# Kernel tuning notes

Measured on AMD Instinct MI355X. Metric: run time of the kernel, lower is better.

The kernel has to match this reference:

```python
import math
import jax, jax.numpy as jnp
import numpy as np

N_HEADS = 32
N_KV_HEADS = 8
HEAD_DIM = 128
DIM = 4096
B = 32
MAX_SEQ = 4096
Q_LEN = 1
START_POS = 4095


def setup_inputs() -> dict:
    key = jax.random.key(0)
    ks = jax.random.split(key, 9)
    x = jax.random.normal(ks[0], (B, Q_LEN, DIM), dtype=jnp.float32)
    # RoPE angles for the current positions (seqlen=Q_LEN, half head_dim pairs)
    inv_freq = 1.0 / (500000.0 ** (np.arange(0, HEAD_DIM, 2, dtype=np.float32) / HEAD_DIM))
    pos = np.arange(START_POS, START_POS + Q_LEN, dtype=np.float32)
    ang = pos[:, None] * inv_freq[None, :]  # [Q_LEN, HEAD_DIM//2]
    freqs_cos = jnp.asarray(np.cos(ang), dtype=jnp.float32)
    freqs_sin = jnp.asarray(np.sin(ang), dtype=jnp.float32)
    cache_k = jax.random.normal(ks[1], (B, MAX_SEQ, N_KV_HEADS, HEAD_DIM), dtype=jnp.float32)
    cache_v = jax.random.normal(ks[2], (B, MAX_SEQ, N_KV_HEADS, HEAD_DIM), dtype=jnp.float32)
    s = 0.02
    wq = jax.random.normal(ks[3], (N_HEADS * HEAD_DIM, DIM), dtype=jnp.float32) * s
    wk = jax.random.normal(ks[4], (N_KV_HEADS * HEAD_DIM, DIM), dtype=jnp.float32) * s
    wv = jax.random.normal(ks[5], (N_KV_HEADS * HEAD_DIM, DIM), dtype=jnp.float32) * s
    wo = jax.random.normal(ks[6], (DIM, N_HEADS * HEAD_DIM), dtype=jnp.float32) * s
    return {"x": x, "start_pos": START_POS, "freqs_cos": freqs_cos, "freqs_sin": freqs_sin,
            "cache_k": cache_k, "cache_v": cache_v, "wq": wq, "wk": wk, "wv": wv, "wo": wo}


def _rope(t, cos, sin):
    # t: [B, S, h, hd]; cos/sin: [S, hd//2]; complex multiply on (even, odd) pairs
    tr = t.reshape(*t.shape[:-1], HEAD_DIM // 2, 2)
    a, b = tr[..., 0], tr[..., 1]
    c = cos[None, :, None, :]
    s = sin[None, :, None, :]
    out = jnp.stack([a * c - b * s, a * s + b * c], axis=-1)
    return out.reshape(t.shape)


def reference(x, start_pos, freqs_cos, freqs_sin, cache_k, cache_v, wq, wk, wv, wo):
    bsz, seqlen, _ = x.shape
    n_rep = N_HEADS // N_KV_HEADS
    xq = jnp.einsum('bsd,od->bso', x, wq).reshape(bsz, seqlen, N_HEADS, HEAD_DIM)
    xk = jnp.einsum('bsd,od->bso', x, wk).reshape(bsz, seqlen, N_KV_HEADS, HEAD_DIM)
    xv = jnp.einsum('bsd,od->bso', x, wv).reshape(bsz, seqlen, N_KV_HEADS, HEAD_DIM)
    xq = _rope(xq, freqs_cos, freqs_sin)
    xk = _rope(xk, freqs_cos, freqs_sin)
    # KV-cache update (start_pos is a static Python int)
    cache_k = cache_k.at[:, start_pos:start_pos + seqlen].set(xk)
    cache_v = cache_v.at[:, start_pos:start_pos + seqlen].set(xv)
    keys = cache_k[:, :start_pos + seqlen]    # [B, T, Hkv, hd]
    values = cache_v[:, :start_pos + seqlen]  # [B, T, Hkv, hd]
    # GQA: group query heads [H] -> [Hkv, n_rep]; avoids materializing repeated KV
    q = xq.reshape(bsz, seqlen, N_KV_HEADS, n_rep, HEAD_DIM)
    scale = 1.0 / math.sqrt(HEAD_DIM)
    scores = jnp.einsum('bsgrd,btgd->bgrst', q, keys) * scale  # [B, Hkv, n_rep, S, T]
    probs = jax.nn.softmax(scores, axis=-1)
    out = jnp.einsum('bgrst,btgd->bsgrd', probs, values)
    out = out.reshape(bsz, seqlen, N_HEADS * HEAD_DIM)
    return jnp.einsum('bse,de->bsd', out, wo)
```

## Files before the change

### kernel.cpp

```cpp
#include <hip/hip_runtime.h>

#define B_    32
#define DIM_  4096
#define NH_   32
#define NKV_  8
#define HD_   128
#define TSEQ  4096
#define NQKV  6144
#define GSPLIT 32
#define BK    32
#define NT    128
#define KRANGE (DIM_ / GSPLIT)
#define KTILES (KRANGE / BK)
#define TSPL  32
#define TS    128

typedef float f4_t __attribute__((ext_vector_type(4)));

__device__ __forceinline__ f4_t ntl(const float* p) {
    return __builtin_nontemporal_load((const f4_t*)p);
}

template<int CTRL>
__device__ __forceinline__ float dpp_add(float x) {
    const int y = __builtin_amdgcn_update_dpp(0, __float_as_int(x),
                                              CTRL, 0xF, 0xF, true);
    return x + __int_as_float(y);
}
__device__ __forceinline__ float red32(float x) {
    x = dpp_add<0xB1>(x);
    x = dpp_add<0x4E>(x);
    x = dpp_add<0x141>(x);
    x = dpp_add<0x140>(x);
    x += __shfl_xor(x, 16);
    return x;
}

__global__ __launch_bounds__(256) void gemm32(
    const float* __restrict__ A, const float* __restrict__ w0,
    const float* __restrict__ w1, const float* __restrict__ w2,
    int b1, int b2, int N, float* __restrict__ po)
{
    __shared__ __align__(16) float wt[BK][NT + 4];
    __shared__ __align__(16) float xp[KRANGE][33];
    const int tid = threadIdx.x;
    const int cg  = tid & 31;
    const int bg  = tid >> 5;
    const int ct  = blockIdx.x * NT;
    const int k0  = blockIdx.y * KRANGE;

    const float* wb_; int c0_;
    if (ct < b1)      { wb_ = w0; c0_ = ct; }
    else if (ct < b2) { wb_ = w1; c0_ = ct - b1; }
    else              { wb_ = w2; c0_ = ct - b2; }

    const int kqx = (tid & 31) * 4;
    const int rrx = tid >> 5;
    const int kq2 = (tid & 7) * 4;
    const int rr2 = tid >> 3;

    f4_t wreg[4];

    #pragma unroll
    for (int st = 0; st < 4; ++st) {
        const int bb = st * 8 + rrx;
        const f4_t xv = *(const f4_t*)(A + (size_t)bb * DIM_ + k0 + kqx);
        xp[kqx + 0][bb] = xv[0]; xp[kqx + 1][bb] = xv[1];
        xp[kqx + 2][bb] = xv[2]; xp[kqx + 3][bb] = xv[3];
    }
    #pragma unroll
    for (int st = 0; st < 4; ++st)
        wreg[st] = ntl(wb_ + (size_t)(c0_ + st * 32 + rr2) * DIM_ + k0 + kq2);
    #pragma unroll
    for (int st = 0; st < 4; ++st) {
        const int c = st * 32 + rr2;
        wt[kq2 + 0][c] = wreg[st][0]; wt[kq2 + 1][c] = wreg[st][1];
        wt[kq2 + 2][c] = wreg[st][2]; wt[kq2 + 3][c] = wreg[st][3];
    }
    __syncthreads();

    float acc[4][4];
    #pragma unroll
    for (int i = 0; i < 4; ++i)
        #pragma unroll
        for (int j = 0; j < 4; ++j) acc[i][j] = 0.f;

    for (int tt = 0; tt < KTILES; ++tt) {
        if (tt < KTILES - 1) {
            #pragma unroll
            for (int st = 0; st < 4; ++st)
                wreg[st] = ntl(wb_ + (size_t)(c0_ + st * 32 + rr2) * DIM_
                               + k0 + (tt + 1) * BK + kq2);
        }
        #pragma unroll 8
        for (int kk = 0; kk < BK; ++kk) {
            const int kr = tt * BK + kk;
            const float4 xa = *(const float4*)&xp[kr][bg * 4];
            const float4 wa = *(const float4*)&wt[kk][cg * 4];
            const float xv[4] = {xa.x, xa.y, xa.z, xa.w};
            const float wv[4] = {wa.x, wa.y, wa.z, wa.w};
            #pragma unroll
            for (int i = 0; i < 4; ++i)
                #pragma unroll
                for (int j = 0; j < 4; ++j)
                    acc[i][j] = fmaf(xv[i], wv[j], acc[i][j]);
        }
        __syncthreads();
        if (tt < KTILES - 1) {
            #pragma unroll
            for (int st = 0; st < 4; ++st) {
                const int c = st * 32 + rr2;
                wt[kq2 + 0][c] = wreg[st][0]; wt[kq2 + 1][c] = wreg[st][1];
                wt[kq2 + 2][c] = wreg[st][2]; wt[kq2 + 3][c] = wreg[st][3];
            }
            __syncthreads();
        }
    }

    const size_t srow = (size_t)blockIdx.y * B_;
    #pragma unroll
    for (int i = 0; i < 4; ++i) {
        const int b = bg * 4 + i;
        const float4 o = make_float4(acc[i][0], acc[i][1], acc[i][2], acc[i][3]);
        *(float4*)&po[(srow + b) * N + ct + cg * 4] = o;
    }
}

__global__ void reduce_rope(const float* __restrict__ po,
                            const float* __restrict__ fc, const float* __restrict__ fs,
                            float* __restrict__ qkv)
{
    const int pid = blockIdx.x * 256 + threadIdx.x;
    const int b  = pid / (NQKV / 4);
    const int c0 = (pid - b * (NQKV / 4)) * 4;
    f4_t v = {0.f, 0.f, 0.f, 0.f};
    #pragma unroll
    for (int s = 0; s < GSPLIT; ++s)
        v += *(const f4_t*)(po + ((size_t)s * B_ + b) * NQKV + c0);
    if (c0 < DIM_ + NKV_ * HD_) {
        const int i = (c0 & 127) >> 1;
        const float ca = fc[i],     sa = fs[i];
        const float cb = fc[i + 1], sb = fs[i + 1];
        f4_t o;
        o[0] = v[0] * ca - v[1] * sa;
        o[1] = v[0] * sa + v[1] * ca;
        o[2] = v[2] * cb - v[3] * sb;
        o[3] = v[2] * sb + v[3] * cb;
        v = o;
    }
    *(f4_t*)(qkv + (size_t)b * NQKV + c0) = v;
}

__device__ __forceinline__ void attn_step(const f4_t kc, const f4_t vc,
                                          const f4_t* q, f4_t* acc, float* l)
{
    float p0 = kc[0]*q[0][0] + kc[1]*q[0][1] + kc[2]*q[0][2] + kc[3]*q[0][3];
    float p1 = kc[0]*q[1][0] + kc[1]*q[1][1] + kc[2]*q[1][2] + kc[3]*q[1][3];
    float p2 = kc[0]*q[2][0] + kc[1]*q[2][1] + kc[2]*q[2][2] + kc[3]*q[2][3];
    float p3 = kc[0]*q[3][0] + kc[1]*q[3][1] + kc[2]*q[3][2] + kc[3]*q[3][3];
    p0 = red32(p0); p1 = red32(p1); p2 = red32(p2); p3 = red32(p3);
    const float scale = 0.08838834764831845f;
    p0 = __expf(p0 * scale); p1 = __expf(p1 * scale);
    p2 = __expf(p2 * scale); p3 = __expf(p3 * scale);
    l[0] += p0; l[1] += p1; l[2] += p2; l[3] += p3;
    acc[0] += p0 * vc; acc[1] += p1 * vc;
    acc[2] += p2 * vc; acc[3] += p3 * vc;
}

__global__ __launch_bounds__(256) void attn_partial(
    const float* __restrict__ qkv, const float* __restrict__ ck,
    const float* __restrict__ cv,
    float* __restrict__ po , float* __restrict__ pl )
{
    const int blk = blockIdx.x;
    const int s = blk & (TSPL - 1);
    const int b = blk / TSPL;
    const int tid  = threadIdx.x;
    const int g    = tid >> 5;
    const int lane = tid & 31;
    const int d4   = lane * 4;
    const float* qb = qkv + (size_t)b * NQKV;

    f4_t q[4];
    #pragma unroll
    for (int h = 0; h < 4; ++h)
        q[h] = *(const f4_t*)(qb + (g * 4 + h) * HD_ + d4);

    f4_t zero4 = {0.f, 0.f, 0.f, 0.f};
    f4_t acc[4] = {zero4, zero4, zero4, zero4};
    float l[4] = {0.f, 0.f, 0.f, 0.f};

    const int t0 = s * TS;
    const bool last = (s == TSPL - 1);
    const int niter = TS - (last ? 1 : 0);

    const size_t base = ((size_t)b * TSEQ + t0) * (NKV_ * HD_) + tid * 4;
    const float* kp = ck + base;
    const float* vp = cv + base;
    const int step = NKV_ * HD_;

    f4_t kc = ntl(kp), vc = ntl(vp);
    kp += step; vp += step;
    f4_t k1 = ntl(kp), v1 = ntl(vp);
    for (int it = 0; it < niter - 2; ++it) {
        kp += step; vp += step;
        const f4_t k2 = ntl(kp);
        const f4_t v2 = ntl(vp);
        attn_step(kc, vc, q, acc, l);
        kc = k1; vc = v1; k1 = k2; v1 = v2;
    }
    attn_step(kc, vc, q, acc, l);
    attn_step(k1, v1, q, acc, l);
    if (last) {
        const f4_t kf = *(const f4_t*)(qb + DIM_ + tid * 4);
        const f4_t vf = *(const f4_t*)(qb + DIM_ + NKV_ * HD_ + tid * 4);
        attn_step(kf, vf, q, acc, l);
    }

    float* pob = po + (((size_t)(b * NKV_ + g) * TSPL) + s) * 512;
    #pragma unroll
    for (int h = 0; h < 4; ++h)
        *(f4_t*)&pob[h * HD_ + d4] = acc[h];
    if (lane == 0) {
        float* plb = pl + ((size_t)(b * NKV_ + g) * TSPL + s) * 4;
        plb[0] = l[0]; plb[1] = l[1]; plb[2] = l[2]; plb[3] = l[3];
    }
}

__global__ void attn_combine(const float* __restrict__ po, const float* __restrict__ pl,
                             float* __restrict__ ao)
{
    const int bg  = blockIdx.x;
    const int tid = threadIdx.x;
    const int e0  = tid * 4;
    const int r   = e0 >> 7;
    f4_t o = {0.f, 0.f, 0.f, 0.f};
    float ls = 0.f;
    #pragma unroll 8
    for (int s = 0; s < TSPL; ++s) {
        o += *(const f4_t*)&po[((size_t)bg * TSPL + s) * 512 + e0];
        ls += pl[((size_t)bg * TSPL + s) * 4 + r];
    }
    o *= (1.f / ls);
    const int b = bg >> 3, g = bg & 7;
    *(f4_t*)&ao[(size_t)b * DIM_ + g * 512 + e0] = o;
}

__global__ void reduce_out(const float* __restrict__ po, float* __restrict__ out)
{
    const int pid = blockIdx.x * 256 + threadIdx.x;
    const int b  = pid >> 10;
    const int c0 = (pid & 1023) * 4;
    f4_t v = {0.f, 0.f, 0.f, 0.f};
    #pragma unroll
    for (int s = 0; s < GSPLIT; ++s)
        v += *(const f4_t*)(po + ((size_t)s * B_ + b) * DIM_ + c0);
    *(f4_t*)(out + (size_t)b * DIM_ + c0) = v;
}

extern "C" void kernel_launch(void* const* d_in, const int* in_sizes, int n_in,
                              void* d_out, int out_size, void* d_ws, size_t ws_size,
                              hipStream_t stream)
{
    (void)in_sizes; (void)n_in; (void)out_size; (void)ws_size;
    const float* x  = (const float*)d_in[0];
    const float* fc = (const float*)d_in[2];
    const float* fs = (const float*)d_in[3];
    const float* ck = (const float*)d_in[4];
    const float* cv = (const float*)d_in[5];
    const float* wq = (const float*)d_in[6];
    const float* wk = (const float*)d_in[7];
    const float* wv = (const float*)d_in[8];
    const float* wo = (const float*)d_in[9];
    float* out = (float*)d_out;
    float* ws  = (float*)d_ws;

    float* qkv  = ws;
    float* aout = ws + 196608;
    float* apo  = ws + 327680;
    float* apl  = ws + 4521984;
    float* gp   = ws + 4554752;

    gemm32<<<dim3(NQKV / NT, GSPLIT), 256, 0, stream>>>(
        x, wq, wk, wv, DIM_, DIM_ + NKV_ * HD_, NQKV, gp);
    reduce_rope<<<dim3(B_ * (NQKV / 4) / 256), 256, 0, stream>>>(gp, fc, fs, qkv);
    attn_partial<<<dim3(B_ * TSPL), 256, 0, stream>>>(qkv, ck, cv, apo, apl);
    attn_combine<<<dim3(B_ * NKV_), 128, 0, stream>>>(apo, apl, aout);
    gemm32<<<dim3(DIM_ / NT, GSPLIT), 256, 0, stream>>>(
        aout, wo, wo, wo, DIM_, DIM_, DIM_, gp);
    reduce_out<<<dim3(B_ * DIM_ / 4 / 256), 256, 0, stream>>>(gp, out);
}
```

Measured before the change: 247.3 us.

## Fuse split-K and attention reductions into producer kernels via last-block atomic counters

Removes the separate reduce_rope, attn_combine and reduce_out kernels. Each producer now increments a per-tile atomic counter, and the last block to arrive performs the cross-split reduction (plus RoPE, or the softmax normalisation) in its epilogue. This cuts kernel launch count and inter-kernel gaps, at the cost of serialised tail work inside a single block per tile and an extra memset for the counters. KRANGE and KTILES are hardcoded to their previous values.

```diff
diff --git a/kernel.cpp b/kernel.cpp
--- a/kernel.cpp
+++ b/kernel.cpp
@@ -2,7 +2,6 @@
 
 #define B_    32
 #define DIM_  4096
-#define NH_   32
 #define NKV_  8
 #define HD_   128
 #define TSEQ  4096
@@ -10,8 +9,8 @@
 #define GSPLIT 32
 #define BK    32
 #define NT    128
-#define KRANGE (DIM_ / GSPLIT)
-#define KTILES (KRANGE / BK)
+#define KRANGE 128
+#define KTILES 4
 #define TSPL  32
 #define TS    128
 
@@ -36,13 +35,30 @@
     return x;
 }
 
-__global__ __launch_bounds__(256) void gemm32(
+__device__ __forceinline__ bool last_block(int* cnt, int total, int* lds_flag) {
+    __syncthreads();
+    if (threadIdx.x == 0) {
+        const int old = __hip_atomic_fetch_add(cnt, 1, __ATOMIC_ACQ_REL,
+                                               __HIP_MEMORY_SCOPE_AGENT);
+        *lds_flag = (old == total - 1);
+    }
+    __syncthreads();
+    if (!*lds_flag) return false;
+    __threadfence();
+    return true;
+}
+
+template<int EPI>
+__global__ __launch_bounds__(256) void gemm_fused(
     const float* __restrict__ A, const float* __restrict__ w0,
     const float* __restrict__ w1, const float* __restrict__ w2,
-    int b1, int b2, int N, float* __restrict__ po)
+    int b1, int b2, int N, float* __restrict__ po,
+    const float* __restrict__ fc, const float* __restrict__ fs,
+    float* __restrict__ dst, int* __restrict__ cnt)
 {
     __shared__ __align__(16) float wt[BK][NT + 4];
     __shared__ __align__(16) float xp[KRANGE][33];
+    __shared__ int lastf;
     const int tid = threadIdx.x;
     const int cg  = tid & 31;
     const int bg  = tid >> 5;
@@ -124,31 +140,35 @@
         const float4 o = make_float4(acc[i][0], acc[i][1], acc[i][2], acc[i][3]);
         *(float4*)&po[(srow + b) * N + ct + cg * 4] = o;
     }
-}
-
-__global__ void reduce_rope(const float* __restrict__ po,
-                            const float* __restrict__ fc, const float* __restrict__ fs,
-                            float* __restrict__ qkv)
-{
-    const int pid = blockIdx.x * 256 + threadIdx.x;
-    const int b  = pid / (NQKV / 4);
-    const int c0 = (pid - b * (NQKV / 4)) * 4;
-    f4_t v = {0.f, 0.f, 0.f, 0.f};
-    #pragma unroll
-    for (int s = 0; s < GSPLIT; ++s)
-        v += *(const f4_t*)(po + ((size_t)s * B_ + b) * NQKV + c0);
-    if (c0 < DIM_ + NKV_ * HD_) {
-        const int i = (c0 & 127) >> 1;
-        const float ca = fc[i],     sa = fs[i];
-        const float cb = fc[i + 1], sb = fs[i + 1];
-        f4_t o;
-        o[0] = v[0] * ca - v[1] * sa;
-        o[1] = v[0] * sa + v[1] * ca;
-        o[2] = v[2] * cb - v[3] * sb;
-        o[3] = v[2] * sb + v[3] * cb;
-        v = o;
-    }
-    *(f4_t*)(qkv + (size_t)b * NQKV + c0) = v;
+
+    if (!last_block(&cnt[blockIdx.x], GSPLIT, &lastf)) return;
+
+    const int m    = tid & 31;
+    const int bsub = tid >> 5;
+    const int c    = ct + m * 4;
+    #pragma unroll
+    for (int p = 0; p < 4; ++p) {
+        const int b = p * 8 + bsub;
+        f4_t v = {0.f, 0.f, 0.f, 0.f};
+        for (int s = 0; s < GSPLIT; ++s)
+            v += *(const f4_t*)(po + ((size_t)s * B_ + b) * N + c);
+        if (EPI == 0) {
+            if (c < DIM_ + NKV_ * HD_) {
+                const int i = (c & 127) >> 1;
+                const float ca = fc[i],     sa = fs[i];
+                const float cb = fc[i + 1], sb = fs[i + 1];
+                f4_t o;
+                o[0] = v[0] * ca - v[1] * sa;
+                o[1] = v[0] * sa + v[1] * ca;
+                o[2] = v[2] * cb - v[3] * sb;
+                o[3] = v[2] * sb + v[3] * cb;
+                v = o;
+            }
+            *(f4_t*)(dst + (size_t)b * NQKV + c) = v;
+        } else {
+            *(f4_t*)(dst + (size_t)b * DIM_ + c) = v;
+        }
+    }
 }
 
 __device__ __forceinline__ void attn_step(const f4_t kc, const f4_t vc,
@@ -167,11 +187,14 @@
     acc[2] += p2 * vc; acc[3] += p3 * vc;
 }
 
-__global__ __launch_bounds__(256) void attn_partial(
+__global__ __launch_bounds__(256) void attn_fused(
     const float* __restrict__ qkv, const float* __restrict__ ck,
     const float* __restrict__ cv,
-    float* __restrict__ po , float* __restrict__ pl )
+    float* __restrict__ apo ,
+    float* __restrict__ apl ,
+    float* __restrict__ aout, int* __restrict__ cnt)
 {
+    __shared__ int lastf;
     const int blk = blockIdx.x;
     const int s = blk & (TSPL - 1);
     const int b = blk / TSPL;
@@ -217,45 +240,34 @@
         attn_step(kf, vf, q, acc, l);
     }
 
-    float* pob = po + (((size_t)(b * NKV_ + g) * TSPL) + s) * 512;
+    float* pob = apo + (((size_t)(b * NKV_ + g) * TSPL) + s) * 512;
     #pragma unroll
     for (int h = 0; h < 4; ++h)
         *(f4_t*)&pob[h * HD_ + d4] = acc[h];
     if (lane == 0) {
-        float* plb = pl + ((size_t)(b * NKV_ + g) * TSPL + s) * 4;
+        float* plb = apl + ((size_t)(b * NKV_ + g) * TSPL + s) * 4;
         plb[0] = l[0]; plb[1] = l[1]; plb[2] = l[2]; plb[3] = l[3];
     }
-}
-
-__global__ void attn_combine(const float* __restrict__ po, const float* __restrict__ pl,
-                             float* __restrict__ ao)
-{
-    const int bg  = blockIdx.x;
-    const int tid = threadIdx.x;
-    const int e0  = tid * 4;
-    const int r   = e0 >> 7;
-    f4_t o = {0.f, 0.f, 0.f, 0.f};
-    float ls = 0.f;
-    #pragma unroll 8
-    for (int s = 0; s < TSPL; ++s) {
-        o += *(const f4_t*)&po[((size_t)bg * TSPL + s) * 512 + e0];
-        ls += pl[((size_t)bg * TSPL + s) * 4 + r];
-    }
-    o *= (1.f / ls);
-    const int b = bg >> 3, g = bg & 7;
-    *(f4_t*)&ao[(size_t)b * DIM_ + g * 512 + e0] = o;
-}
-
-__global__ void reduce_out(const float* __restrict__ po, float* __restrict__ out)
-{
-    const int pid = blockIdx.x * 256 + threadIdx.x;
-    const int b  = pid >> 10;
-    const int c0 = (pid & 1023) * 4;
-    f4_t v = {0.f, 0.f, 0.f, 0.f};
-    #pragma unroll
-    for (int s = 0; s < GSPLIT; ++s)
-        v += *(const f4_t*)(po + ((size_t)s * B_ + b) * DIM_ + c0);
-    *(f4_t*)(out + (size_t)b * DIM_ + c0) = v;
+
+    if (!last_block(&cnt[b], TSPL, &lastf)) return;
+
+    #pragma unroll
+    for (int p = 0; p < 4; ++p) {
+        const int flat = p * 256 + tid;
+        const int gg = flat >> 7;
+        const int mm = flat & 127;
+        const int hh = mm >> 5;
+        const int dd = (mm & 31) * 4;
+        const size_t pb = (size_t)(b * NKV_ + gg) * TSPL;
+        f4_t o = zero4;
+        float ls = 0.f;
+        for (int s2 = 0; s2 < TSPL; ++s2) {
+            o += *(const f4_t*)(apo + (pb + s2) * 512 + hh * HD_ + dd);
+            ls += apl[(pb + s2) * 4 + hh];
+        }
+        o *= (1.f / ls);
+        *(f4_t*)(aout + (size_t)b * DIM_ + gg * 512 + hh * HD_ + dd) = o;
+    }
 }
 
 extern "C" void kernel_launch(void* const* d_in, const int* in_sizes, int n_in,
@@ -280,13 +292,13 @@
     float* apo  = ws + 327680;
     float* apl  = ws + 4521984;
     float* gp   = ws + 4554752;
-
-    gemm32<<<dim3(NQKV / NT, GSPLIT), 256, 0, stream>>>(
-        x, wq, wk, wv, DIM_, DIM_ + NKV_ * HD_, NQKV, gp);
-    reduce_rope<<<dim3(B_ * (NQKV / 4) / 256), 256, 0, stream>>>(gp, fc, fs, qkv);
-    attn_partial<<<dim3(B_ * TSPL), 256, 0, stream>>>(qkv, ck, cv, apo, apl);
-    attn_combine<<<dim3(B_ * NKV_), 128, 0, stream>>>(apo, apl, aout);
-    gemm32<<<dim3(DIM_ / NT, GSPLIT), 256, 0, stream>>>(
-        aout, wo, wo, wo, DIM_, DIM_, DIM_, gp);
-    reduce_out<<<dim3(B_ * DIM_ / 4 / 256), 256, 0, stream>>>(gp, out);
-}
+    int*   cnt  = (int*)(ws + 10846208);
+
+    hipMemsetAsync(cnt, 0, 128 * sizeof(int), stream);
+    gemm_fused<0><<<dim3(NQKV / NT, GSPLIT), 256, 0, stream>>>(
+        x, wq, wk, wv, DIM_, DIM_ + NKV_ * HD_, NQKV, gp, fc, fs, qkv, cnt);
+    attn_fused<<<dim3(B_ * TSPL), 256, 0, stream>>>(
+        qkv, ck, cv, apo, apl, aout, cnt + 64);
+    gemm_fused<1><<<dim3(DIM_ / NT, GSPLIT), 256, 0, stream>>>(
+        aout, wo, wo, wo, DIM_, DIM_, DIM_, gp, nullptr, nullptr, out, cnt + 96);
+}
```

Result: slower. 453.4 us (+83.3%).
